# Kernel optimization log

Hardware: AMD Instinct MI355X
Metric: run time of the kernel (lower is better)

Reference implementation:

```python
import jax, jax.numpy as jnp
import numpy as np

TAU = 2.0
V_TH = 1.0
SG_ALPHA = 4.0  # spikingjelly surrogate.Sigmoid default

@jax.custom_vjp
def spike_fn(u):
    # heaviside(u) with sigmoid surrogate gradient; u = v - v_threshold
    return (u >= 0.0).astype(u.dtype)

def _spike_fwd(u):
    return spike_fn(u), u

def _spike_bwd(u, g):
    s = jax.nn.sigmoid(SG_ALPHA * u)
    return (g * SG_ALPHA * s * (1.0 - s),)

spike_fn.defvjp(_spike_fwd, _spike_bwd)

def lif_scan(h):
    # h: [T, B, D] input currents; multi-step LIF with hard reset to 0,
    # decay_input=True: v = v + (h - v) / tau
    def step(v, h_t):
        v = v + (h_t - v) / TAU
        s = spike_fn(v - V_TH)
        v = v * (1.0 - jax.lax.stop_gradient(s))  # detach_reset=True, v_reset=0
        return v, s
    v0 = jnp.zeros_like(h[0])
    _, spikes = jax.lax.scan(step, v0, h)
    return spikes  # [T, B, D]

def setup_inputs() -> dict:
    key = jax.random.key(0)
    k_x, k_w1, k_b1, k_w2, k_b2 = jax.random.split(key, 5)
    T, B, D, C = 32, 512, 1024, 1000
    lim1 = 1.0 / np.sqrt(D)
    return {
        "x": jax.random.normal(k_x, (T, B, D), dtype=jnp.float32),
        "W1": jax.random.uniform(k_w1, (D, D), jnp.float32, -lim1, lim1),
        "b1": jax.random.uniform(k_b1, (D,), jnp.float32, -lim1, lim1),
        "W2": jax.random.uniform(k_w2, (C, D), jnp.float32, -lim1, lim1),
        "b2": jax.random.uniform(k_b2, (C,), jnp.float32, -lim1, lim1),
    }

def reference(x, W1, b1, W2, b2):
    # linear_1: [T,B,D] @ [D,D]^T + b1
    h = jnp.einsum('tbd,ed->tbe', x, W1) + b1
    s = lif_scan(h)                               # [T,B,D] spikes in {0,1}
    y = jnp.einsum('tbd,cd->tbc', s, W2) + b2     # [T,B,C]
    y = y.mean(axis=0)                            # [B,C]
    return jax.nn.log_softmax(y, axis=1)
```

## Files before the change

### kernel.cpp

```cpp
#include <hip/hip_runtime.h>
#include <math.h>

#define T_STEPS 32
#define B_SZ    512
#define D_SZ    1024
#define C_SZ    1000
#define KZ      8
#define HP      132

typedef __bf16 bf16x8 __attribute__((ext_vector_type(8)));
typedef float  f32x4  __attribute__((ext_vector_type(4)));

__device__ __forceinline__ unsigned short f2bf(float f) {
    unsigned u = __float_as_uint(f);
    unsigned r = u + 0x7FFFu + ((u >> 16) & 1u);
    return (unsigned short)(r >> 16);
}
__device__ __forceinline__ float bf2f(unsigned short b) {
    return __uint_as_float(((unsigned)b) << 16);
}

__device__ __forceinline__ void async_copy16(const void* g, void* l) {
    __builtin_amdgcn_global_load_lds(
        (const __attribute__((address_space(1))) unsigned int*)g,
        (__attribute__((address_space(3))) unsigned int*)l,
        16, 0, 0);
}

__device__ __forceinline__ bf16x8 cvt8(const float4 u, const float4 v) {
    bf16x8 r;
    r[0] = (__bf16)u.x; r[1] = (__bf16)u.y; r[2] = (__bf16)u.z; r[3] = (__bf16)u.w;
    r[4] = (__bf16)v.x; r[5] = (__bf16)v.y; r[6] = (__bf16)v.z; r[7] = (__bf16)v.w;
    return r;
}

#define NX4   4194304
#define NW14  262144
#define NW24  256000
#define NWTOT (NW14 + NW24)
#define NCTOT (NX4 + NW14 + NW24)

__global__ __launch_bounds__(256) void cast_all_k(
    const float* __restrict__ X,  unsigned short* __restrict__ X_bf,
    const float* __restrict__ W1, unsigned short* __restrict__ W1_bf,
    const float* __restrict__ W2, unsigned short* __restrict__ W2_bf)
{
    const int idx = blockIdx.x * 256 + threadIdx.x;
    const float4* s; ushort4* d; int j;
    if (idx < NX4)              { s = (const float4*)X;  d = (ushort4*)X_bf;  j = idx; }
    else if (idx < NX4 + NW14)  { s = (const float4*)W1; d = (ushort4*)W1_bf; j = idx - NX4; }
    else                        { s = (const float4*)W2; d = (ushort4*)W2_bf; j = idx - NX4 - NW14; }
    const float4 v = s[j];
    ushort4 o;
    o.x = f2bf(v.x); o.y = f2bf(v.y); o.z = f2bf(v.z); o.w = f2bf(v.w);
    d[j] = o;
}

__global__ __launch_bounds__(256) void cast_w_k(
    const float* __restrict__ W1, unsigned short* __restrict__ W1_bf,
    const float* __restrict__ W2, unsigned short* __restrict__ W2_bf)
{
    const int idx = blockIdx.x * 256 + threadIdx.x;
    const float4* s; ushort4* d; int j;
    if (idx < NW14) { s = (const float4*)W1; d = (ushort4*)W1_bf; j = idx; }
    else            { s = (const float4*)W2; d = (ushort4*)W2_bf; j = idx - NW14; }
    const float4 v = s[j];
    ushort4 o;
    o.x = f2bf(v.x); o.y = f2bf(v.y); o.z = f2bf(v.z); o.w = f2bf(v.w);
    d[j] = o;
}

__global__ __launch_bounds__(256) void gemm1_scan_bf_k(
    const unsigned short* __restrict__ Xb, const unsigned short* __restrict__ Bm,
    const float* __restrict__ bias, unsigned short* __restrict__ cnt)
{
    __shared__ __align__(16) unsigned short smem[32768];

    const int tid  = threadIdx.x;
    const int wave = tid >> 6;
    const int lane = tid & 63;
    const int lm   = lane & 15;
    const int quad = lane >> 4;
    const int wm   = (wave >> 1) * 64;
    const int wn   = (wave & 1) * 64;

    const int f  = blockIdx.x;
    const int rr = f >> 9;
    const int cc = f & 7;
    const int ss = (f >> 3) & 63;
    const int xb = ss & 7;
    const int yb = rr * 64 + (ss >> 3) * 8 + cc;
    const int b0 = yb * 4;
    const int n0 = xb * 128;

    f32x4 acc[4][4];
    #pragma unroll
    for (int i = 0; i < 4; ++i)
        #pragma unroll
        for (int j = 0; j < 4; ++j)
            acc[i][j] = (f32x4){0.f, 0.f, 0.f, 0.f};

    int srow[4], sgq[4];
    size_t aoff[4];
    unsigned ldsoff[4];
    #pragma unroll
    for (int p = 0; p < 4; ++p) {
        const int s = p * 256 + tid;
        const int rho = s >> 3;
        srow[p] = rho;
        sgq[p]  = (s & 7) ^ (rho & 7);
        aoff[p] = (size_t)((rho >> 2) * 512 + b0 + (rho & 3)) * D_SZ;
        ldsoff[p] = (unsigned)(p * 256 + wave * 64) * 16u;
    }
    const int fq0 = quad ^ (lm & 7);

#define STAGE(buf_, k0_) do {                                                    \
        char* abase = (char*)smem + (buf_) * 16384;                              \
        char* bbase = (char*)smem + 32768 + (buf_) * 16384;                      \
        _Pragma("unroll")                                                        \
        for (int p = 0; p < 4; ++p)                                              \
            async_copy16(Xb + aoff[p] + (k0_) + sgq[p] * 8,                      \
                         abase + ldsoff[p]);                                     \
        _Pragma("unroll")                                                        \
        for (int p = 0; p < 4; ++p)                                              \
            async_copy16(Bm + (size_t)(n0 + srow[p]) * D_SZ + (k0_) + sgq[p] * 8,\
                         bbase + ldsoff[p]);                                     \
    } while (0)

#define COMPUTE(buf_) do {                                                       \
        const bf16x8* Ar = (const bf16x8*)((char*)smem + (buf_) * 16384);        \
        const bf16x8* Br = (const bf16x8*)((char*)smem + 32768 + (buf_) * 16384);\
        __builtin_amdgcn_s_setprio(1);                                           \
        _Pragma("unroll")                                                        \
        for (int kk = 0; kk < 2; ++kk) {                                         \
            const int fqk = fq0 ^ (kk * 4);                                      \
            bf16x8 af[4], bfr[4];                                                \
            _Pragma("unroll")                                                    \
            for (int i2 = 0; i2 < 4; ++i2) {                                     \
                af[i2]  = Ar[(wm + i2 * 16 + lm) * 8 + fqk];                     \
                bfr[i2] = Br[(wn + i2 * 16 + lm) * 8 + fqk];                     \
            }                                                                    \
            _Pragma("unroll")                                                    \
            for (int mi = 0; mi < 4; ++mi)                                       \
                _Pragma("unroll")                                                \
                for (int ni = 0; ni < 4; ++ni)                                   \
                    acc[mi][ni] = __builtin_amdgcn_mfma_f32_16x16x32_bf16(       \
                        af[mi], bfr[ni], acc[mi][ni], 0, 0, 0);                  \
        }                                                                        \
        __builtin_amdgcn_s_setprio(0);                                           \
    } while (0)

    STAGE(0, 0);
    __syncthreads();

    for (int t = 0; t < 14; t += 2) {
        STAGE(1, (t + 1) * 64);
        COMPUTE(0);
        __syncthreads();
        STAGE(0, (t + 2) * 64);
        COMPUTE(1);
        __syncthreads();
    }
    STAGE(1, 15 * 64);
    COMPUTE(0);
    __syncthreads();
    COMPUTE(1);
    __syncthreads();

#undef STAGE
#undef COMPUTE

    #pragma unroll
    for (int ni = 0; ni < 4; ++ni) {
        const int nn = wn + ni * 16 + lm;
        const float bv = bias[n0 + nn];
        #pragma unroll
        for (int mi = 0; mi < 4; ++mi) {
            const f32x4 v = acc[mi][ni];
            #pragma unroll
            for (int r = 0; r < 4; ++r)
                smem[(wm + mi * 16 + quad * 4 + r) * HP + nn] = f2bf(v[r] + bv);
        }
    }
    __syncthreads();

    {
        const unsigned* smemU = (const unsigned*)smem;
        const int bb = tid >> 6;
        const int c2 = tid & 63;
        float v0 = 0.f, cv0 = 0.f, v1 = 0.f, cv1 = 0.f;
        #pragma unroll
        for (int t = 0; t < T_STEPS; ++t) {
            const unsigned u = smemU[(t * 4 + bb) * (HP / 2) + c2];
            const float h0 = bf2f((unsigned short)(u & 0xFFFFu));
            const float h1 = bf2f((unsigned short)(u >> 16));
            v0 = 0.5f * (v0 + h0);
            const float s0 = (v0 >= 1.0f) ? 1.0f : 0.0f;
            cv0 += s0; v0 *= (1.0f - s0);
            v1 = 0.5f * (v1 + h1);
            const float s1 = (v1 >= 1.0f) ? 1.0f : 0.0f;
            cv1 += s1; v1 *= (1.0f - s1);
        }
        ushort2 o;
        o.x = f2bf(cv0); o.y = f2bf(cv1);
        *(ushort2*)&cnt[(size_t)(b0 + bb) * D_SZ + n0 + 2 * c2] = o;
    }
}

__global__ __launch_bounds__(256) void gemm1_scan_f32_k(
    const float* __restrict__ X, const unsigned short* __restrict__ Bm,
    const float* __restrict__ bias, unsigned short* __restrict__ cnt)
{
    __shared__ __align__(16) unsigned short smem[32768];

    const int tid  = threadIdx.x;
    const int wave = tid >> 6;
    const int lane = tid & 63;
    const int lm   = lane & 15;
    const int quad = lane >> 4;
    const int wm   = (wave >> 1) * 64;
    const int wn   = (wave & 1) * 64;

    const int f  = blockIdx.x;
    const int rr = f >> 9;
    const int cc = f & 7;
    const int ss = (f >> 3) & 63;
    const int xb = ss & 7;
    const int yb = rr * 64 + (ss >> 3) * 8 + cc;
    const int b0 = yb * 4;
    const int n0 = xb * 128;

    f32x4 acc[4][4];
    #pragma unroll
    for (int i = 0; i < 4; ++i)
        #pragma unroll
        for (int j = 0; j < 4; ++j)
            acc[i][j] = (f32x4){0.f, 0.f, 0.f, 0.f};

    int srow[4], sgq[4];
    size_t arowoff[4];
    unsigned ldsoffB[4];
    #pragma unroll
    for (int p = 0; p < 4; ++p) {
        const int s = p * 256 + tid;
        const int rho = s >> 3;
        srow[p] = rho;
        sgq[p]  = (s & 7) ^ (rho & 7);
        arowoff[p] = (size_t)((rho >> 2) * 512 + b0 + (rho & 3)) * D_SZ;
        ldsoffB[p] = (unsigned)(p * 256 + wave * 64) * 16u;
    }
    const int fq0 = quad ^ (lm & 7);

    float4 au[4], av[4];

#define LOAD_A(k0_) do {                                                        \
        _Pragma("unroll")                                                       \
        for (int p = 0; p < 4; ++p) {                                           \
            const float* srcp = X + arowoff[p] + (k0_) + sgq[p] * 8;            \
            au[p] = *(const float4*)(srcp);                                     \
            av[p] = *(const float4*)(srcp + 4);                                 \
        }                                                                       \
    } while (0)

#define STAGE_B(buf_, k0_) do {                                                 \
        char* bdst = (char*)(smem + 16384 + (buf_) * 8192);                     \
        _Pragma("unroll")                                                       \
        for (int p = 0; p < 4; ++p)                                             \
            async_copy16(Bm + (size_t)(n0 + srow[p]) * D_SZ + (k0_) + sgq[p] * 8,\
                         bdst + ldsoffB[p]);                                    \
    } while (0)

#define WRITE_A(buf_) do {                                                      \
        bf16x8* adst = (bf16x8*)(smem + (buf_) * 8192);                         \
        _Pragma("unroll")                                                       \
        for (int p = 0; p < 4; ++p)                                             \
            adst[p * 256 + tid] = cvt8(au[p], av[p]);                           \
    } while (0)

#define COMPUTE(buf_) do {                                                      \
        const bf16x8* Ar = (const bf16x8*)(smem + (buf_) * 8192);               \
        const bf16x8* Br = (const bf16x8*)(smem + 16384 + (buf_) * 8192);       \
        __builtin_amdgcn_s_setprio(1);                                          \
        _Pragma("unroll")                                                       \
        for (int kk = 0; kk < 2; ++kk) {                                        \
            const int fqk = fq0 ^ (kk * 4);                                     \
            bf16x8 af[4], bfr[4];                                               \
            _Pragma("unroll")                                                   \
            for (int i2 = 0; i2 < 4; ++i2) {                                    \
                af[i2]  = Ar[(wm + i2 * 16 + lm) * 8 + fqk];                    \
                bfr[i2] = Br[(wn + i2 * 16 + lm) * 8 + fqk];                    \
            }                                                                   \
            _Pragma("unroll")                                                   \
            for (int mi = 0; mi < 4; ++mi)                                      \
                _Pragma("unroll")                                               \
                for (int ni = 0; ni < 4; ++ni)                                  \
                    acc[mi][ni] = __builtin_amdgcn_mfma_f32_16x16x32_bf16(      \
                        af[mi], bfr[ni], acc[mi][ni], 0, 0, 0);                 \
        }                                                                       \
        __builtin_amdgcn_s_setprio(0);                                          \
    } while (0)

    LOAD_A(0);
    STAGE_B(0, 0);
    WRITE_A(0);
    __syncthreads();
    LOAD_A(64);
    STAGE_B(1, 64);

    for (int i = 0; i < 14; i += 2) {
        COMPUTE(0);
        WRITE_A(1);
        __syncthreads();
        LOAD_A((i + 2) * 64);
        STAGE_B(0, (i + 2) * 64);

        COMPUTE(1);
        WRITE_A(0);
        __syncthreads();
        LOAD_A((i + 3) * 64);
        STAGE_B(1, (i + 3) * 64);
    }
    COMPUTE(0);
    WRITE_A(1);
    __syncthreads();
    COMPUTE(1);
    __syncthreads();

#undef LOAD_A
#undef STAGE_B
#undef WRITE_A
#undef COMPUTE

    #pragma unroll
    for (int ni = 0; ni < 4; ++ni) {
        const int nn = wn + ni * 16 + lm;
        const float bv = bias[n0 + nn];
        #pragma unroll
        for (int mi = 0; mi < 4; ++mi) {
            const f32x4 v = acc[mi][ni];
            #pragma unroll
            for (int r = 0; r < 4; ++r)
                smem[(wm + mi * 16 + quad * 4 + r) * HP + nn] = f2bf(v[r] + bv);
        }
    }
    __syncthreads();

    {
        const unsigned* smemU = (const unsigned*)smem;
        const int bb = tid >> 6;
        const int c2 = tid & 63;
        float v0 = 0.f, cv0 = 0.f, v1 = 0.f, cv1 = 0.f;
        #pragma unroll
        for (int t = 0; t < T_STEPS; ++t) {
            const unsigned u = smemU[(t * 4 + bb) * (HP / 2) + c2];
            const float h0 = bf2f((unsigned short)(u & 0xFFFFu));
            const float h1 = bf2f((unsigned short)(u >> 16));
            v0 = 0.5f * (v0 + h0);
            const float s0 = (v0 >= 1.0f) ? 1.0f : 0.0f;
            cv0 += s0; v0 *= (1.0f - s0);
            v1 = 0.5f * (v1 + h1);
            const float s1 = (v1 >= 1.0f) ? 1.0f : 0.0f;
            cv1 += s1; v1 *= (1.0f - s1);
        }
        ushort2 o;
        o.x = f2bf(cv0); o.y = f2bf(cv1);
        *(ushort2*)&cnt[(size_t)(b0 + bb) * D_SZ + n0 + 2 * c2] = o;
    }
}

__global__ __launch_bounds__(256) void gemm2_splitk_k(
    const unsigned short* __restrict__ A, const unsigned short* __restrict__ Bm,
    float* __restrict__ partial)
{
    __shared__ __align__(16) unsigned short As[128 * 32];
    __shared__ __align__(16) unsigned short Bs[128 * 32];

    const int tid  = threadIdx.x;
    const int wave = tid >> 6;
    const int lane = tid & 63;
    const int lm   = lane & 15;
    const int quad = lane >> 4;
    const int wm   = (wave >> 1) * 64;
    const int wn   = (wave & 1) * 64;
    const int n0   = blockIdx.x * 128;
    const int m0   = blockIdx.y * 128;
    const int kz   = blockIdx.z;

    f32x4 acc[4][4];
    #pragma unroll
    for (int i = 0; i < 4; ++i)
        #pragma unroll
        for (int j = 0; j < 4; ++j)
            acc[i][j] = (f32x4){0.f, 0.f, 0.f, 0.f};

    int srow[2], sgq[2];
    unsigned ldsoff[2];
    #pragma unroll
    for (int p = 0; p < 2; ++p) {
        const int s = p * 256 + tid;
        srow[p] = s >> 2;
        sgq[p]  = (s & 3) ^ ((srow[p] >> 1) & 3);
        ldsoff[p] = (unsigned)(p * 256 + wave * 64) * 16u;
    }
    const int fq = quad ^ ((lm >> 1) & 3);

    const int kbeg = kz * (D_SZ / KZ);
    for (int k0 = kbeg; k0 < kbeg + D_SZ / KZ; k0 += 32) {
        #pragma unroll
        for (int p = 0; p < 2; ++p) {
            async_copy16(A + (size_t)(m0 + srow[p]) * D_SZ + k0 + sgq[p] * 8,
                         (char*)As + ldsoff[p]);
            int brow = n0 + srow[p];
            if (brow > C_SZ - 1) brow = C_SZ - 1;
            async_copy16(Bm + (size_t)brow * D_SZ + k0 + sgq[p] * 8,
                         (char*)Bs + ldsoff[p]);
        }
        __syncthreads();

        bf16x8 af[4], bfr[4];
        #pragma unroll
        for (int i = 0; i < 4; ++i) {
            af[i]  = ((const bf16x8*)As)[(wm + i * 16 + lm) * 4 + fq];
            bfr[i] = ((const bf16x8*)Bs)[(wn + i * 16 + lm) * 4 + fq];
        }
        #pragma unroll
        for (int mi = 0; mi < 4; ++mi)
            #pragma unroll
            for (int ni = 0; ni < 4; ++ni)
                acc[mi][ni] = __builtin_amdgcn_mfma_f32_16x16x32_bf16(
                    af[mi], bfr[ni], acc[mi][ni], 0, 0, 0);
        __syncthreads();
    }

    #pragma unroll
    for (int ni = 0; ni < 4; ++ni) {
        const int nn = n0 + wn + ni * 16 + lm;
        if (nn >= C_SZ) continue;
        #pragma unroll
        for (int mi = 0; mi < 4; ++mi) {
            const f32x4 v = acc[mi][ni];
            #pragma unroll
            for (int r = 0; r < 4; ++r) {
                const int mm = m0 + wm + mi * 16 + quad * 4 + r;
                partial[((size_t)kz * B_SZ + mm) * C_SZ + nn] = v[r];
            }
        }
    }
}

__global__ __launch_bounds__(256) void reduce_lsm_k(
    const float* __restrict__ partial, const float* __restrict__ b2,
    float* __restrict__ out)
{
    __shared__ float red_max[4];
    __shared__ float red_sum[4];

    const int b   = blockIdx.x;
    const int tid = threadIdx.x;

    float vals[4];
    float m = -1e30f;
    #pragma unroll
    for (int k = 0; k < 4; ++k) {
        const int c = tid + k * 256;
        if (c < C_SZ) {
            float s = 0.f;
            #pragma unroll
            for (int z = 0; z < KZ; ++z)
                s += partial[((size_t)z * B_SZ + b) * C_SZ + c];
            vals[k] = s * (1.0f / (float)T_STEPS) + b2[c];
        } else {
            vals[k] = -1e30f;
        }
        m = fmaxf(m, vals[k]);
    }
    #pragma unroll
    for (int off = 32; off > 0; off >>= 1)
        m = fmaxf(m, __shfl_down(m, off, 64));
    const int wave = tid >> 6;
    const int lane = tid & 63;
    if (lane == 0) red_max[wave] = m;
    __syncthreads();
    m = fmaxf(fmaxf(red_max[0], red_max[1]), fmaxf(red_max[2], red_max[3]));

    float s = 0.f;
    #pragma unroll
    for (int k = 0; k < 4; ++k) {
        const int c = tid + k * 256;
        if (c < C_SZ) s += __expf(vals[k] - m);
    }
    #pragma unroll
    for (int off = 32; off > 0; off >>= 1)
        s += __shfl_down(s, off, 64);
    if (lane == 0) red_sum[wave] = s;
    __syncthreads();
    s = red_sum[0] + red_sum[1] + red_sum[2] + red_sum[3];

    const float lse = m + logf(s);
    #pragma unroll
    for (int k = 0; k < 4; ++k) {
        const int c = tid + k * 256;
        if (c < C_SZ) out[(size_t)b * C_SZ + c] = vals[k] - lse;
    }
}

extern "C" void kernel_launch(void* const* d_in, const int* in_sizes, int n_in,
                              void* d_out, int out_size, void* d_ws, size_t ws_size,
                              hipStream_t stream)
{
    const float* x  = (const float*)d_in[0];
    const float* W1 = (const float*)d_in[1];
    const float* b1 = (const float*)d_in[2];
    const float* W2 = (const float*)d_in[3];
    const float* b2 = (const float*)d_in[4];
    float* out = (float*)d_out;

    char* ws = (char*)d_ws;

    if (ws_size >= 38748160u) {
        unsigned short* X_bf    = (unsigned short*)(ws);
        float*          partial = (float*)(ws);
        unsigned short* W1_bf   = (unsigned short*)(ws + 33554432);
        unsigned short* W2_bf   = (unsigned short*)(ws + 35651584);
        unsigned short* cnt_bf  = (unsigned short*)(ws + 37699584);

        cast_all_k<<<NCTOT / 256, 256, 0, stream>>>(x, X_bf, W1, W1_bf, W2, W2_bf);
        gemm1_scan_bf_k<<<(B_SZ / 4) * (D_SZ / 128), 256, 0, stream>>>(
            X_bf, W1_bf, b1, cnt_bf);
        {
            dim3 grid((C_SZ + 127) / 128, B_SZ / 128, KZ);
            gemm2_splitk_k<<<grid, 256, 0, stream>>>(cnt_bf, W2_bf, partial);
        }
        reduce_lsm_k<<<B_SZ, 256, 0, stream>>>(partial, b2, out);
    } else {
        unsigned short* W1_bf   = (unsigned short*)(ws);
        unsigned short* W2_bf   = (unsigned short*)(ws + 2097152);
        unsigned short* cnt_bf  = (unsigned short*)(ws + 4145152);
        float*          partial = (float*)(ws + 5193728);

        cast_w_k<<<NWTOT / 256, 256, 0, stream>>>(W1, W1_bf, W2, W2_bf);
        gemm1_scan_f32_k<<<(B_SZ / 4) * (D_SZ / 128), 256, 0, stream>>>(
            x, W1_bf, b1, cnt_bf);
        {
            dim3 grid((C_SZ + 127) / 128, B_SZ / 128, KZ);
            gemm2_splitk_k<<<grid, 256, 0, stream>>>(cnt_bf, W2_bf, partial);
        }
        reduce_lsm_k<<<B_SZ, 256, 0, stream>>>(partial, b2, out);
    }
}
```

Measured before the change: 160.6 us.

## Enlarge GEMM1+scan tile to 256x256 with 8 waves and interleaved staging

Replaces the 128x128, 4-wave fused GEMM1+LIF-scan kernel with a 256x256 tile run by 512 threads (8 waves, 8x4 MFMA accumulators per wave). Global-to-LDS prefetch of the next K slice is split into A and B halves, interleaved with MFMA phases separated by barriers. The epilogue uses an XOR-swizzled LDS layout instead of padding. The larger tile raises arithmetic intensity and cuts redundant X/W1 loads. In exchange it launches only 256 workgroups, raises register pressure, uses 128 KB of LDS, and adds barriers.

```diff
diff --git a/kernel.cpp b/kernel.cpp
--- a/kernel.cpp
+++ b/kernel.cpp
@@ -70,140 +70,170 @@
     d[j] = o;
 }
 
-__global__ __launch_bounds__(256) void gemm1_scan_bf_k(
+__global__ __launch_bounds__(512, 2) void gemm1_scan256_k(
     const unsigned short* __restrict__ Xb, const unsigned short* __restrict__ Bm,
     const float* __restrict__ bias, unsigned short* __restrict__ cnt)
 {
-    __shared__ __align__(16) unsigned short smem[32768];
+    __shared__ __align__(16) unsigned short smem[65536];
 
     const int tid  = threadIdx.x;
     const int wave = tid >> 6;
     const int lane = tid & 63;
     const int lm   = lane & 15;
     const int quad = lane >> 4;
-    const int wm   = (wave >> 1) * 64;
-    const int wn   = (wave & 1) * 64;
-
-    const int f  = blockIdx.x;
-    const int rr = f >> 9;
-    const int cc = f & 7;
-    const int ss = (f >> 3) & 63;
-    const int xb = ss & 7;
-    const int yb = rr * 64 + (ss >> 3) * 8 + cc;
-    const int b0 = yb * 4;
-    const int n0 = xb * 128;
-
-    f32x4 acc[4][4];
-    #pragma unroll
-    for (int i = 0; i < 4; ++i)
+    const int wm   = (wave >> 2) * 128;
+    const int wn   = (wave & 3) * 64;
+
+    const int wgid = (blockIdx.x & 7) * 32 + (blockIdx.x >> 3);
+    const int yb = wgid >> 2;
+    const int xb = wgid & 3;
+    const int b0 = yb * 8;
+    const int n0 = xb * 256;
+
+    f32x4 acc[8][4];
+    #pragma unroll
+    for (int i = 0; i < 8; ++i)
         #pragma unroll
         for (int j = 0; j < 4; ++j)
             acc[i][j] = (f32x4){0.f, 0.f, 0.f, 0.f};
 
-    int srow[4], sgq[4];
-    size_t aoff[4];
-    unsigned ldsoff[4];
+    size_t aoff[4], boff[4];
+    unsigned ldsoffp[4];
     #pragma unroll
     for (int p = 0; p < 4; ++p) {
-        const int s = p * 256 + tid;
+        const int s   = p * 512 + tid;
         const int rho = s >> 3;
-        srow[p] = rho;
-        sgq[p]  = (s & 7) ^ (rho & 7);
-        aoff[p] = (size_t)((rho >> 2) * 512 + b0 + (rho & 3)) * D_SZ;
-        ldsoff[p] = (unsigned)(p * 256 + wave * 64) * 16u;
+        const int gq  = (s & 7) ^ (rho & 7);
+        aoff[p] = (size_t)((rho >> 3) * 512 + b0 + (rho & 7)) * D_SZ + gq * 8;
+        boff[p] = (size_t)(n0 + rho) * D_SZ + gq * 8;
+        ldsoffp[p] = (unsigned)(p * 512 + wave * 64) * 16u;
     }
     const int fq0 = quad ^ (lm & 7);
 
-#define STAGE(buf_, k0_) do {                                                    \
-        char* abase = (char*)smem + (buf_) * 16384;                              \
-        char* bbase = (char*)smem + 32768 + (buf_) * 16384;                      \
+#define STG_A(cb_, k0_) do {                                                     \
+        char* ab_ = (char*)smem + (cb_) * 32768;                                 \
         _Pragma("unroll")                                                        \
         for (int p = 0; p < 4; ++p)                                              \
-            async_copy16(Xb + aoff[p] + (k0_) + sgq[p] * 8,                      \
-                         abase + ldsoff[p]);                                     \
+            async_copy16(Xb + aoff[p] + (k0_), ab_ + ldsoffp[p]);                \
+    } while (0)
+
+#define STG_B(cb_, k0_) do {                                                     \
+        char* bb_ = (char*)smem + 65536 + (cb_) * 32768;                         \
         _Pragma("unroll")                                                        \
         for (int p = 0; p < 4; ++p)                                              \
-            async_copy16(Bm + (size_t)(n0 + srow[p]) * D_SZ + (k0_) + sgq[p] * 8,\
-                         bbase + ldsoff[p]);                                     \
-    } while (0)
-
-#define COMPUTE(buf_) do {                                                       \
-        const bf16x8* Ar = (const bf16x8*)((char*)smem + (buf_) * 16384);        \
-        const bf16x8* Br = (const bf16x8*)((char*)smem + 32768 + (buf_) * 16384);\
+            async_copy16(Bm + boff[p] + (k0_), bb_ + ldsoffp[p]);                \
+    } while (0)
+
+#define READ_A(mi0_) do {                                                        \
+        _Pragma("unroll")                                                        \
+        for (int m2 = 0; m2 < 2; ++m2) {                                         \
+            const int rw_ = wm + ((mi0_) + m2) * 16 + lm;                        \
+            af[m2][0] = Ar[rw_ * 8 + fq0];                                       \
+            af[m2][1] = Ar[rw_ * 8 + (fq0 ^ 4)];                                 \
+        }                                                                        \
+    } while (0)
+
+#define MFMA2(mi0_) do {                                                         \
         __builtin_amdgcn_s_setprio(1);                                           \
         _Pragma("unroll")                                                        \
-        for (int kk = 0; kk < 2; ++kk) {                                         \
-            const int fqk = fq0 ^ (kk * 4);                                      \
-            bf16x8 af[4], bfr[4];                                                \
+        for (int kk = 0; kk < 2; ++kk)                                           \
             _Pragma("unroll")                                                    \
-            for (int i2 = 0; i2 < 4; ++i2) {                                     \
-                af[i2]  = Ar[(wm + i2 * 16 + lm) * 8 + fqk];                     \
-                bfr[i2] = Br[(wn + i2 * 16 + lm) * 8 + fqk];                     \
-            }                                                                    \
-            _Pragma("unroll")                                                    \
-            for (int mi = 0; mi < 4; ++mi)                                       \
+            for (int m2 = 0; m2 < 2; ++m2)                                       \
                 _Pragma("unroll")                                                \
                 for (int ni = 0; ni < 4; ++ni)                                   \
-                    acc[mi][ni] = __builtin_amdgcn_mfma_f32_16x16x32_bf16(       \
-                        af[mi], bfr[ni], acc[mi][ni], 0, 0, 0);                  \
-        }                                                                        \
+                    acc[(mi0_) + m2][ni] = __builtin_amdgcn_mfma_f32_16x16x32_bf16( \
+                        af[m2][kk], bfr[ni][kk], acc[(mi0_) + m2][ni], 0, 0, 0); \
         __builtin_amdgcn_s_setprio(0);                                           \
     } while (0)
 
-    STAGE(0, 0);
-    __syncthreads();
-
-    for (int t = 0; t < 14; t += 2) {
-        STAGE(1, (t + 1) * 64);
-        COMPUTE(0);
+    STG_A(0, 0);
+    STG_B(0, 0);
+    __syncthreads();
+
+    #pragma unroll 2
+    for (int t = 0; t < 16; ++t) {
+        const int c  = t & 1;
+        const bf16x8* Ar = (const bf16x8*)((const char*)smem + c * 32768);
+        const bf16x8* Br = (const bf16x8*)((const char*)smem + 65536 + c * 32768);
+        const int kn = (t + 1) * 64;
+        bf16x8 bfr[4][2], af[2][2];
+
+        #pragma unroll
+        for (int ni = 0; ni < 4; ++ni) {
+            const int rw = (wn + ni * 16 + lm) * 8;
+            bfr[ni][0] = Br[rw + fq0];
+            bfr[ni][1] = Br[rw + (fq0 ^ 4)];
+        }
+        READ_A(0);
+        if (t < 15) STG_A(c ^ 1, kn);
+        __builtin_amdgcn_s_barrier();
+        MFMA2(0);
+        __builtin_amdgcn_s_barrier();
+
+        READ_A(2);
+        if (t < 15) STG_B(c ^ 1, kn);
+        __builtin_amdgcn_s_barrier();
+        MFMA2(2);
+        __builtin_amdgcn_s_barrier();
+
+        READ_A(4);
+        __builtin_amdgcn_s_barrier();
+        MFMA2(4);
+        __builtin_amdgcn_s_barrier();
+
+        READ_A(6);
+        __builtin_amdgcn_s_barrier();
+        MFMA2(6);
         __syncthreads();
-        STAGE(0, (t + 2) * 64);
-        COMPUTE(1);
-        __syncthreads();
-    }
-    STAGE(1, 15 * 64);
-    COMPUTE(0);
-    __syncthreads();
-    COMPUTE(1);
-    __syncthreads();
-
-#undef STAGE
-#undef COMPUTE
+    }
+
+#undef STG_A
+#undef STG_B
+#undef READ_A
+#undef MFMA2
 
     #pragma unroll
     for (int ni = 0; ni < 4; ++ni) {
-        const int nn = wn + ni * 16 + lm;
-        const float bv = bias[n0 + nn];
-        #pragma unroll
-        for (int mi = 0; mi < 4; ++mi) {
+        const int col = wn + ni * 16 + lm;
+        const float bv = bias[n0 + col];
+        #pragma unroll
+        for (int mi = 0; mi < 8; ++mi) {
             const f32x4 v = acc[mi][ni];
             #pragma unroll
-            for (int r = 0; r < 4; ++r)
-                smem[(wm + mi * 16 + quad * 4 + r) * HP + nn] = f2bf(v[r] + bv);
+            for (int q = 0; q < 4; ++q) {
+                const int row = wm + mi * 16 + quad * 4 + q;
+                smem[row * 256 + (col ^ (((row >> 2) & 3) << 4))] = f2bf(v[q] + bv);
+            }
         }
     }
     __syncthreads();
 
     {
         const unsigned* smemU = (const unsigned*)smem;
-        const int bb = tid >> 6;
-        const int c2 = tid & 63;
-        float v0 = 0.f, cv0 = 0.f, v1 = 0.f, cv1 = 0.f;
-        #pragma unroll
-        for (int t = 0; t < T_STEPS; ++t) {
-            const unsigned u = smemU[(t * 4 + bb) * (HP / 2) + c2];
-            const float h0 = bf2f((unsigned short)(u & 0xFFFFu));
-            const float h1 = bf2f((unsigned short)(u >> 16));
-            v0 = 0.5f * (v0 + h0);
-            const float s0 = (v0 >= 1.0f) ? 1.0f : 0.0f;
-            cv0 += s0; v0 *= (1.0f - s0);
-            v1 = 0.5f * (v1 + h1);
-            const float s1 = (v1 >= 1.0f) ? 1.0f : 0.0f;
-            cv1 += s1; v1 *= (1.0f - s1);
-        }
-        ushort2 o;
-        o.x = f2bf(cv0); o.y = f2bf(cv1);
-        *(ushort2*)&cnt[(size_t)(b0 + bb) * D_SZ + n0 + 2 * c2] = o;
+        const int uc = tid & 127;
+        const int h4 = tid >> 7;
+        #pragma unroll
+        for (int g = 0; g < 2; ++g) {
+            const int bb = h4 + g * 4;
+            float v0 = 0.f, cv0 = 0.f, v1 = 0.f, cv1 = 0.f;
+            #pragma unroll
+            for (int t2 = 0; t2 < T_STEPS; ++t2) {
+                const int rho = t2 * 8 + bb;
+                const unsigned u =
+                    smemU[rho * 128 + (uc ^ (((rho >> 2) & 3) << 3))];
+                const float h0 = bf2f((unsigned short)(u & 0xFFFFu));
+                const float h1 = bf2f((unsigned short)(u >> 16));
+                v0 = 0.5f * (v0 + h0);
+                const float s0 = (v0 >= 1.0f) ? 1.0f : 0.0f;
+                cv0 += s0; v0 *= (1.0f - s0);
+                v1 = 0.5f * (v1 + h1);
+                const float s1 = (v1 >= 1.0f) ? 1.0f : 0.0f;
+                cv1 += s1; v1 *= (1.0f - s1);
+            }
+            ushort2 o;
+            o.x = f2bf(cv0); o.y = f2bf(cv1);
+            *(ushort2*)&cnt[(size_t)(b0 + bb) * D_SZ + n0 + 2 * uc] = o;
+        }
     }
 }
 
@@ -339,8 +369,8 @@
         for (int mi = 0; mi < 4; ++mi) {
             const f32x4 v = acc[mi][ni];
             #pragma unroll
-            for (int r = 0; r < 4; ++r)
-                smem[(wm + mi * 16 + quad * 4 + r) * HP + nn] = f2bf(v[r] + bv);
+            for (int q = 0; q < 4; ++q)
+                smem[(wm + mi * 16 + quad * 4 + q) * HP + nn] = f2bf(v[q] + bv);
         }
     }
     __syncthreads();
@@ -440,9 +470,9 @@
         for (int mi = 0; mi < 4; ++mi) {
             const f32x4 v = acc[mi][ni];
             #pragma unroll
-            for (int r = 0; r < 4; ++r) {
-                const int mm = m0 + wm + mi * 16 + quad * 4 + r;
-                partial[((size_t)kz * B_SZ + mm) * C_SZ + nn] = v[r];
+            for (int q = 0; q < 4; ++q) {
+                const int mm = m0 + wm + mi * 16 + quad * 4 + q;
+                partial[((size_t)kz * B_SZ + mm) * C_SZ + nn] = v[q];
             }
         }
     }
@@ -525,8 +555,7 @@
         unsigned short* cnt_bf  = (unsigned short*)(ws + 37699584);
 
         cast_all_k<<<NCTOT / 256, 256, 0, stream>>>(x, X_bf, W1, W1_bf, W2, W2_bf);
-        gemm1_scan_bf_k<<<(B_SZ / 4) * (D_SZ / 128), 256, 0, stream>>>(
-            X_bf, W1_bf, b1, cnt_bf);
+        gemm1_scan256_k<<<256, 512, 0, stream>>>(X_bf, W1_bf, b1, cnt_bf);
         {
             dim3 grid((C_SZ + 127) / 128, B_SZ / 128, KZ);
             gemm2_splitk_k<<<grid, 256, 0, stream>>>(cnt_bf, W2_bf, partial);
```

Result: faster. 152.2 us (-5.2%).
